# Kernel optimization log

Measured on AMD Instinct MI355X. Metric: run time of the kernel, lower is better.

The kernel has to match this reference:

```python
import jax, jax.numpy as jnp
import numpy as np

HEADS = 8
DIM_HEAD = 128
SCALE = DIM_HEAD ** -0.5
EPS = 1e-5


def layer_norm(t, w, b):
    mu = t.mean(-1, keepdims=True)
    var = ((t - mu) ** 2).mean(-1, keepdims=True)
    return (t - mu) * jax.lax.rsqrt(var + EPS) * w + b


def setup_inputs() -> dict:
    key = jax.random.key(0)
    ks = jax.random.split(key, 8)
    b, n, dim = 4, 1024, 1024
    inner = HEADS * DIM_HEAD  # 1024
    w = 0.02
    return {
        "x": jax.random.normal(ks[0], (b, n, dim), jnp.float32),
        "cond_info": jax.random.normal(ks[1], (b, n, dim), jnp.float32),
        "ref": jax.random.normal(ks[2], (b, n, dim), jnp.float32),
        "ln_w": jnp.ones((dim,), jnp.float32),
        "ln_b": jnp.zeros((dim,), jnp.float32),
        "cln_w": jnp.ones((dim,), jnp.float32),
        "cln_b": jnp.zeros((dim,), jnp.float32),
        "Wk": jax.random.normal(ks[3], (3 * dim, inner), jnp.float32) * w,
        "Wv": jax.random.normal(ks[4], (2 * dim, inner), jnp.float32) * w,
        "Wo": jax.random.normal(ks[5], (inner, dim), jnp.float32) * w,
        "bo": jnp.zeros((dim,), jnp.float32),
        "th_w": jax.random.normal(ks[6], (HEADS, HEADS), jnp.float32) * 0.3,
        "cth_w": jax.random.normal(ks[7], (HEADS, HEADS), jnp.float32) * 0.3,
    }


def reference(x, cond_info, ref, ln_w, ln_b, cln_w, cln_b, Wk, Wv, Wo, bo, th_w, cth_w):
    b, n, _ = x.shape
    h, d = HEADS, DIM_HEAD
    xn = layer_norm(x, ln_w, ln_b)
    rn = layer_norm(ref, ln_w, ln_b)
    cn = layer_norm(cond_info, cln_w, cln_b)
    # projections (y_to_q output is unused in the original forward; omitted)
    cond = jnp.concatenate([xn, cn, rn], axis=-1) @ Wk   # [b, n, h*d]
    refv = jnp.concatenate([xn, rn], axis=-1) @ Wv       # [b, n, h*d]
    split = lambda t: t.reshape(b, n, h, d).transpose(0, 2, 1, 3)  # b h n d
    cond, refv = split(cond), split(refv)
    sim = jnp.einsum('bhid,bhjd->bhij', cond, refv) * SCALE
    attn = jax.nn.softmax(sim, axis=-1)           # row softmax
    context_attn = jax.nn.softmax(sim, axis=-2)   # column softmax
    # talking heads: 1x1 conv over head dim, weight [out_h, in_h]
    attn = jnp.einsum('gh,bhij->bgij', th_w, attn)
    context_attn = jnp.einsum('gh,bhij->bgij', cth_w, context_attn)
    out = jnp.einsum('bhij,bhjd->bhid', attn, refv)
    context_out = jnp.einsum('bhji,bhjd->bhid', context_attn, cond)
    merge = lambda t: t.transpose(0, 2, 1, 3).reshape(b, n, h * d)
    out = merge(out) @ Wo + bo
    context_out = merge(context_out)
    return out, context_out
```

## Files before the change

kernel.cpp:

```cpp
#include <hip/hip_runtime.h>
#include <hip/hip_bf16.h>
#include <stdint.h>

typedef unsigned short u16;
typedef __attribute__((ext_vector_type(8))) short bf16x8;
typedef __attribute__((ext_vector_type(4))) float f32x4;

#define HEADS 8
#define DHEAD 128
#define NSEQ 1024
#define BATCH 4
#define DIM 1024
#define ATT_SCALE 0.088388347648318447f

static __device__ __forceinline__ float bf2f(u16 u){
  union { unsigned int i; float f; } c; c.i = ((unsigned int)u) << 16; return c.f;
}
static __device__ __forceinline__ u16 f2bf(float f){
  union { float f; unsigned int i; } c; c.f = f;
  unsigned int x = c.i;
  return (u16)((x + 0x7fffu + ((x >> 16) & 1u)) >> 16);
}

static __device__ __forceinline__ void gload_lds16(const void* g, void* l){
  __builtin_amdgcn_global_load_lds((__attribute__((address_space(1))) void*)(g),
                                   (__attribute__((address_space(3))) void*)(l),
                                   16, 0, 0);
}

__global__ __launch_bounds__(256)
void ln_kernel(const float* __restrict__ x, const float* __restrict__ w,
               const float* __restrict__ b, u16* __restrict__ out)
{
  const int row = blockIdx.x;
  const int t = threadIdx.x;
  const float* xr = x + (size_t)row * DIM;
  float4 v4 = *(const float4*)(xr + t*4);
  float v[4] = {v4.x, v4.y, v4.z, v4.w};
  float s = v[0]+v[1]+v[2]+v[3];
  __shared__ float red[256];
  red[t] = s; __syncthreads();
  for (int o=128;o;o>>=1){ if (t<o) red[t]+=red[t+o]; __syncthreads(); }
  const float mean = red[0] * (1.0f/DIM);
  __syncthreads();
  s = 0.f;
#pragma unroll
  for (int i=0;i<4;i++){ float d = v[i]-mean; s += d*d; }
  red[t] = s; __syncthreads();
  for (int o=128;o;o>>=1){ if (t<o) red[t]+=red[t+o]; __syncthreads(); }
  const float rstd = rsqrtf(red[0]*(1.0f/DIM) + 1e-5f);
  float4 w4 = *(const float4*)(w + t*4);
  float4 b4 = *(const float4*)(b + t*4);
  float wv[4] = {w4.x, w4.y, w4.z, w4.w};
  float bv[4] = {b4.x, b4.y, b4.z, b4.w};
  union { uint2 u; u16 s[4]; } ov;
#pragma unroll
  for (int i=0;i<4;i++)
    ov.s[i] = f2bf((v[i]-mean)*rstd*wv[i] + bv[i]);
  *(uint2*)(out + (size_t)row*DIM + t*4) = ov.u;
}

__global__ __launch_bounds__(256)
void wcvt_kernel(const float* __restrict__ Wk, const float* __restrict__ Wv,
                 const float* __restrict__ Wo,
                 u16* __restrict__ WkT, u16* __restrict__ WvT, u16* __restrict__ WoT)
{
  const int z = blockIdx.z;
  const int K = (z==0) ? 3072 : (z==1) ? 2048 : 1024;
  if ((int)blockIdx.x*32 >= K) return;
  const float* W = (z==0) ? Wk : (z==1) ? Wv : Wo;
  u16* WT = (z==0) ? WkT : (z==1) ? WvT : WoT;
  __shared__ float tile[32][33];
  const int k0 = blockIdx.x*32, n0 = blockIdx.y*32;
  const int t = threadIdx.x, tc = t&31, tr = t>>5;
#pragma unroll
  for (int p=0;p<4;p++)
    tile[tr+p*8][tc] = W[(size_t)(k0+tr+p*8)*DIM + n0+tc];
  __syncthreads();
#pragma unroll
  for (int p=0;p<4;p++)
    WT[(size_t)(n0+tr+p*8)*K + k0+tc] = f2bf(tile[tc][tr+p*8]);
}

__global__ __launch_bounds__(256)
void gemm_kernel(const u16* __restrict__ A0, const u16* __restrict__ A1,
                 const u16* __restrict__ A2, const u16* __restrict__ A0b,
                 const u16* __restrict__ A1b,
                 const u16* __restrict__ B1, const u16* __restrict__ B2,
                 void* __restrict__ Cv, void* __restrict__ Cv2,
                 const float* __restrict__ bias,
                 int K1, int K2, int lda, int ldb1, int ldb2, int ldc,
                 long a_plane, long b_plane, long c_plane,
                 int epi1, int epi2, int z_split, float alpha)
{
  __shared__ __attribute__((aligned(16))) u16 sA[2][4096];
  __shared__ __attribute__((aligned(16))) u16 sB[2][4096];
  const int t = threadIdx.x;
  const int m0 = blockIdx.y*128, n0 = blockIdx.x*128;
  const int zz = blockIdx.z;
  const bool side = (zz >= z_split);
  const int z = side ? (zz - z_split) : zz;
  const u16* a0 = (side ? A0b : A0) + (size_t)z*a_plane;
  const u16* a1 = (side ? A1b : A1) + (size_t)z*a_plane;
  const u16* a2 = A2 + (size_t)z*a_plane;
  const u16* bB = (side ? B2 : B1) + (size_t)z*b_plane;
  void* Cp = side ? Cv2 : Cv;
  const int EPI = side ? epi2 : epi1;
  const int K   = side ? K2 : K1;
  const int ldb = side ? ldb2 : ldb1;

  const int wave = t>>6, lane = t&63;
  const int wm = (wave>>1)*64, wn = (wave&1)*64;
  const int lm = lane&15, q = lane>>4;

  const f32x4 zero4 = {0.f,0.f,0.f,0.f};
  f32x4 acc[4][4];
#pragma unroll
  for (int i=0;i<4;i++)
#pragma unroll
    for (int j=0;j<4;j++) acc[i][j] = zero4;

  const int arowblk = wave*32;

  const int KT = K >> 5;

  auto issueA = [&](int kt, int buf){
    const int kg = kt<<5, seg = kg>>10, ka = kg&1023;
    const u16* Ap = (seg==0) ? a0 : (seg==1 ? a1 : a2);
#pragma unroll
    for (int rr=0; rr<2; ++rr){
      const int rb = arowblk + rr*16;
      gload_lds16(Ap + (size_t)(m0+rb+lm)*lda + (ka + q*8), &sA[buf][rb*32]);
    }
  };
  auto issueB = [&](int kt, int buf){
    const int kg = kt<<5;
#pragma unroll
    for (int rr=0; rr<2; ++rr){
      const int rb = arowblk + rr*16;
      gload_lds16(bB + (size_t)(n0+rb+lm)*ldb + (kg + q*8), &sB[buf][rb*32]);
    }
  };

  issueA(0, 0);
  issueB(0, 0);

  int cur = 0;
  for (int kt=0; kt<KT; ++kt){
    __syncthreads();
    if (kt+1 < KT){
      issueA(kt+1, cur^1);
      issueB(kt+1, cur^1);
    }
    bf16x8 af[4], bfr[4];
#pragma unroll
    for (int f=0; f<4; ++f){
      af[f]  = *(const bf16x8*)&sA[cur][((wm>>4)+f)*512 + lane*8];
      bfr[f] = *(const bf16x8*)&sB[cur][((wn>>4)+f)*512 + lane*8];
    }
#pragma unroll
    for (int fm=0; fm<4; ++fm)
#pragma unroll
      for (int fn=0; fn<4; ++fn)
        acc[fm][fn] = __builtin_amdgcn_mfma_f32_16x16x32_bf16(af[fm], bfr[fn], acc[fm][fn], 0, 0, 0);
    cur ^= 1;
  }

#pragma unroll
  for (int fm=0; fm<4; ++fm){
#pragma unroll
    for (int fn=0; fn<4; ++fn){
#pragma unroll
      for (int r=0; r<4; ++r){
        const int m = m0 + wm + fm*16 + q*4 + r;
        const int n = n0 + wn + fn*16 + lm;
        float val = acc[fm][fn][r] * alpha;
        if (EPI == 0){
          ((u16*)Cp)[(size_t)z*c_plane + (size_t)m*ldc + n] = f2bf(val);
        } else if (EPI == 1){
          ((u16*)Cp)[((size_t)(z>>3)*NSEQ + m)*DIM + (size_t)(z&7)*DHEAD + n] = f2bf(val);
        } else if (EPI == 2){
          ((float*)Cp)[(size_t)m*ldc + n] = val + bias[n];
        } else if (EPI == 3){
          ((u16*)Cp)[(size_t)(((m>>10)*HEADS + (n>>7))*NSEQ + (m&1023))*DHEAD + (n&127)] = f2bf(val);
        } else {
          ((float*)Cp)[((size_t)(z>>3)*NSEQ + m)*DIM + (size_t)(z&7)*DHEAD + n] = val;
        }
      }
    }
  }
}

__global__ __launch_bounds__(256)
void transpose_kernel(const u16* __restrict__ X, u16* __restrict__ XT)
{
  __shared__ u16 tile[32][33];
  const int z = blockIdx.z;
  const int i0 = blockIdx.y*32, d0 = blockIdx.x*32;
  const int t = threadIdx.x;
  const int tc = t & 31, tr = t >> 5;
  const u16* Xp = X + (size_t)z*NSEQ*DHEAD;
#pragma unroll
  for (int p=0;p<4;p++){
    int i = tr + p*8;
    tile[i][tc] = Xp[(size_t)(i0+i)*DHEAD + d0 + tc];
  }
  __syncthreads();
  u16* Op = XT + (size_t)z*DHEAD*NSEQ;
#pragma unroll
  for (int p=0;p<4;p++){
    int d = tr + p*8;
    Op[(size_t)(d0+d)*NSEQ + i0 + tc] = tile[tc][d];
  }
}

__global__ __launch_bounds__(256)
void row_stats_kernel(const u16* __restrict__ sim,
                      float* __restrict__ rmax, float* __restrict__ rrcp)
{
  const int wave = threadIdx.x >> 6, lane = threadIdx.x & 63;
  const int row = blockIdx.x*4 + wave;
  const u16* sr = sim + (size_t)row * NSEQ;
  float v[16]; float m = -1e30f;
#pragma unroll
  for (int c=0;c<16;c++){ v[c] = bf2f(sr[lane + c*64]); m = fmaxf(m, v[c]); }
#pragma unroll
  for (int off=32; off; off>>=1) m = fmaxf(m, __shfl_xor(m, off));
  float s = 0.f;
#pragma unroll
  for (int c=0;c<16;c++) s += __expf(v[c]-m);
#pragma unroll
  for (int off=32; off; off>>=1) s += __shfl_xor(s, off);
  if (lane == 0){ rmax[row] = m; rrcp[row] = 1.0f/s; }
}

__global__ __launch_bounds__(256)
void col_stats_kernel(const u16* __restrict__ sim,
                      float* __restrict__ cmax, float* __restrict__ crcp)
{
  __shared__ float smx[4][64], ssm[4][64];
  const int t = threadIdx.x;
  const int jl = t & 63, slice = t >> 6;
  const int c = blockIdx.x*64 + jl;
  const int bh = c >> 10, j = c & 1023;
  const u16* sp = sim + (size_t)bh*NSEQ*NSEQ + j + (size_t)(slice*256)*NSEQ;
  float m = -1e30f, s = 0.f;
  for (int i=0;i<256;i++){
    float v = bf2f(sp[(size_t)i*NSEQ]);
    float nm = fmaxf(m, v);
    s = s*__expf(m-nm) + __expf(v-nm);
    m = nm;
  }
  smx[slice][jl] = m; ssm[slice][jl] = s;
  __syncthreads();
  if (slice == 0){
    float M = smx[0][jl];
#pragma unroll
    for (int p=1;p<4;p++) M = fmaxf(M, smx[p][jl]);
    float S = 0.f;
#pragma unroll
    for (int p=0;p<4;p++) S += ssm[p][jl]*__expf(smx[p][jl]-M);
    cmax[c] = M; crcp[c] = 1.0f/S;
  }
}

__global__ __launch_bounds__(256)
void mix_kernel(u16* simam,
                const float* __restrict__ rmax, const float* __restrict__ rrcp,
                const float* __restrict__ cmax, const float* __restrict__ crcp,
                const float* __restrict__ thw, const float* __restrict__ cthw,
                u16* __restrict__ cmT)
{
  __shared__ float s_th[64], s_cth[64];
  __shared__ u16 s_cm[8][32][33];
  const int t = threadIdx.x;
  if (t < 64){ s_th[t] = thw[t]; s_cth[t] = cthw[t]; }
  __syncthreads();
  const int b = blockIdx.z, i0 = blockIdx.y*32, j0 = blockIdx.x*32;
  const int tj = t & 31, ti = t >> 5;
  for (int p=0;p<4;p++){
    const int i = ti + p*8;
    float a[8], c[8];
#pragma unroll
    for (int h=0;h<8;h++){
      const int bh = b*8 + h;
      const float v = bf2f(simam[((size_t)bh*NSEQ + (i0+i))*NSEQ + j0 + tj]);
      a[h] = __expf(v - rmax[(size_t)bh*NSEQ + i0+i]) * rrcp[(size_t)bh*NSEQ + i0+i];
      c[h] = __expf(v - cmax[(size_t)bh*NSEQ + j0+tj]) * crcp[(size_t)bh*NSEQ + j0+tj];
    }
#pragma unroll
    for (int g=0;g<8;g++){
      float sa = 0.f, sc = 0.f;
#pragma unroll
      for (int h=0;h<8;h++){ sa += s_th[g*8+h]*a[h]; sc += s_cth[g*8+h]*c[h]; }
      simam[((size_t)(b*8+g)*NSEQ + (i0+i))*NSEQ + j0 + tj] = f2bf(sa);
      s_cm[g][i][tj] = f2bf(sc);
    }
  }
  __syncthreads();
#pragma unroll
  for (int g=0;g<8;g++){
#pragma unroll
    for (int p=0;p<4;p++){
      const int j = ti + p*8;
      cmT[((size_t)(b*8+g)*NSEQ + (j0+j))*NSEQ + i0 + tj] = s_cm[g][tj][j];
    }
  }
}

extern "C" void kernel_launch(void* const* d_in, const int* in_sizes, int n_in,
                              void* d_out, int out_size, void* d_ws, size_t ws_size,
                              hipStream_t stream)
{
  const float* x     = (const float*)d_in[0];
  const float* cinfo = (const float*)d_in[1];
  const float* ref   = (const float*)d_in[2];
  const float* ln_w  = (const float*)d_in[3];
  const float* ln_b  = (const float*)d_in[4];
  const float* cln_w = (const float*)d_in[5];
  const float* cln_b = (const float*)d_in[6];
  const float* Wk    = (const float*)d_in[7];
  const float* Wv    = (const float*)d_in[8];
  const float* Wo    = (const float*)d_in[9];
  const float* bo    = (const float*)d_in[10];
  const float* thw   = (const float*)d_in[11];
  const float* cthw  = (const float*)d_in[12];
  float* out = (float*)d_out;

  char* ws = (char*)d_ws;
  u16* xn    = (u16*)(ws + 0);
  u16* cn    = (u16*)(ws + 8388608);
  u16* rn    = (u16*)(ws + 16777216);
  u16* cond  = (u16*)(ws + 25165824);
  u16* refv  = (u16*)(ws + 33554432);
  u16* condT = (u16*)(ws + 41943040);
  u16* refvT = (u16*)(ws + 50331648);
  u16* sim   = (u16*)(ws + 58720256);
  u16* cmT   = (u16*)(ws + 125829120);
  u16* WkT   = (u16*)(ws + 192937984);
  u16* WvT   = (u16*)(ws + 199229440);
  u16* WoT   = (u16*)(ws + 203423744);
  float* rmax = (float*)(ws + 8388608);
  float* rrcp = (float*)(ws + 8388608 + 131072);
  float* cmax = (float*)(ws + 8388608 + 262144);
  float* crcp = (float*)(ws + 8388608 + 393216);
  u16* out_pre = (u16*)(ws + 0);

  ln_kernel<<<4096, 256, 0, stream>>>(x,     ln_w,  ln_b,  xn);
  ln_kernel<<<4096, 256, 0, stream>>>(ref,   ln_w,  ln_b,  rn);
  ln_kernel<<<4096, 256, 0, stream>>>(cinfo, cln_w, cln_b, cn);

  wcvt_kernel<<<dim3(96,32,3), 256, 0, stream>>>(Wk, Wv, Wo, WkT, WvT, WoT);

  gemm_kernel<<<dim3(8,32,2), 256, 0, stream>>>(
      xn, cn, rn, xn, rn, WkT, WvT, cond, refv, nullptr,
      3072, 2048, DIM, 3072, 2048, 0, 0, 0, 0, 3, 3, 1, 1.0f);

  transpose_kernel<<<dim3(4,32,32), 256, 0, stream>>>(cond, condT);
  transpose_kernel<<<dim3(4,32,32), 256, 0, stream>>>(refv, refvT);

  gemm_kernel<<<dim3(8,8,32), 256, 0, stream>>>(
      cond, cond, cond, cond, cond, refv, refv, sim, sim, nullptr,
      DHEAD, DHEAD, DHEAD, DHEAD, DHEAD, NSEQ,
      (long)NSEQ*DHEAD, (long)NSEQ*DHEAD, (long)NSEQ*NSEQ, 0, 0, 1000000, ATT_SCALE);

  row_stats_kernel<<<8192, 256, 0, stream>>>(sim, rmax, rrcp);
  col_stats_kernel<<<512, 256, 0, stream>>>(sim, cmax, crcp);

  mix_kernel<<<dim3(32,32,4), 256, 0, stream>>>(sim, rmax, rrcp, cmax, crcp, thw, cthw, cmT);

  gemm_kernel<<<dim3(1,8,64), 256, 0, stream>>>(
      sim, sim, sim, cmT, cmT, refvT, condT, out_pre, out + (size_t)BATCH*NSEQ*DIM, nullptr,
      1024, 1024, NSEQ, NSEQ, NSEQ, 0,
      (long)NSEQ*NSEQ, (long)DHEAD*NSEQ, 0, 1, 4, 32, 1.0f);

  gemm_kernel<<<dim3(8,32,1), 256, 0, stream>>>(
      out_pre, out_pre, out_pre, out_pre, out_pre, WoT, WoT, out, out, bo,
      1024, 1024, DIM, 1024, 1024, DIM, 0, 0, 0, 2, 2, 1000000, 1.0f);
}
```

Measured before the change: 472.8 us.

## Store attention matrices and transposed values in k-panel layout for PV gemm

The mix kernel now writes the mixed row-attention and column-attention matrices into a separate buffer in a k-panelled layout (32-column panels stored contiguously), and the transpose kernel writes condT/refvT the same way. A templated PANEL gemm path then loads each 32-wide k-slice as a contiguous block instead of strided rows, aiming to improve load coalescing and cache locality in the large attention-times-value gemm. Workspace is reshuffled so WoT is converted later into the freed sim region, which adds an extra kernel launch and relies on the aliasing being correct.

```diff
diff --git a/kernel.cpp b/kernel.cpp
--- a/kernel.cpp
+++ b/kernel.cpp
@@ -61,15 +61,8 @@
 }
 
 __global__ __launch_bounds__(256)
-void wcvt_kernel(const float* __restrict__ Wk, const float* __restrict__ Wv,
-                 const float* __restrict__ Wo,
-                 u16* __restrict__ WkT, u16* __restrict__ WvT, u16* __restrict__ WoT)
-{
-  const int z = blockIdx.z;
-  const int K = (z==0) ? 3072 : (z==1) ? 2048 : 1024;
-  if ((int)blockIdx.x*32 >= K) return;
-  const float* W = (z==0) ? Wk : (z==1) ? Wv : Wo;
-  u16* WT = (z==0) ? WkT : (z==1) ? WvT : WoT;
+void wcvt_kernel(const float* __restrict__ W, u16* __restrict__ WT, int K)
+{
   __shared__ float tile[32][33];
   const int k0 = blockIdx.x*32, n0 = blockIdx.y*32;
   const int t = threadIdx.x, tc = t&31, tr = t>>5;
@@ -82,6 +75,7 @@
     WT[(size_t)(n0+tr+p*8)*K + k0+tc] = f2bf(tile[tc][tr+p*8]);
 }
 
+template<bool PANEL>
 __global__ __launch_bounds__(256)
 void gemm_kernel(const u16* __restrict__ A0, const u16* __restrict__ A1,
                  const u16* __restrict__ A2, const u16* __restrict__ A0b,
@@ -125,20 +119,39 @@
   const int KT = K >> 5;
 
   auto issueA = [&](int kt, int buf){
-    const int kg = kt<<5, seg = kg>>10, ka = kg&1023;
-    const u16* Ap = (seg==0) ? a0 : (seg==1 ? a1 : a2);
-#pragma unroll
-    for (int rr=0; rr<2; ++rr){
-      const int rb = arowblk + rr*16;
-      gload_lds16(Ap + (size_t)(m0+rb+lm)*lda + (ka + q*8), &sA[buf][rb*32]);
+    const int kg = kt<<5;
+    if (PANEL){
+#pragma unroll
+      for (int rr=0; rr<2; ++rr){
+        const int rb = arowblk + rr*16;
+        gload_lds16(a0 + (size_t)(kg>>5)*32768 + (size_t)(m0+rb+lm)*32 + q*8,
+                    &sA[buf][rb*32]);
+      }
+    } else {
+      const int seg = kg>>10, ka = kg&1023;
+      const u16* Ap = (seg==0) ? a0 : (seg==1 ? a1 : a2);
+#pragma unroll
+      for (int rr=0; rr<2; ++rr){
+        const int rb = arowblk + rr*16;
+        gload_lds16(Ap + (size_t)(m0+rb+lm)*lda + (ka + q*8), &sA[buf][rb*32]);
+      }
     }
   };
   auto issueB = [&](int kt, int buf){
     const int kg = kt<<5;
-#pragma unroll
-    for (int rr=0; rr<2; ++rr){
-      const int rb = arowblk + rr*16;
-      gload_lds16(bB + (size_t)(n0+rb+lm)*ldb + (kg + q*8), &sB[buf][rb*32]);
+    if (PANEL){
+#pragma unroll
+      for (int rr=0; rr<2; ++rr){
+        const int rb = arowblk + rr*16;
+        gload_lds16(bB + (size_t)(kg>>5)*4096 + (size_t)(n0+rb+lm)*32 + q*8,
+                    &sB[buf][rb*32]);
+      }
+    } else {
+#pragma unroll
+      for (int rr=0; rr<2; ++rr){
+        const int rb = arowblk + rr*16;
+        gload_lds16(bB + (size_t)(n0+rb+lm)*ldb + (kg + q*8), &sB[buf][rb*32]);
+      }
     }
   };
 
@@ -210,7 +223,7 @@
 #pragma unroll
   for (int p=0;p<4;p++){
     int d = tr + p*8;
-    Op[(size_t)(d0+d)*NSEQ + i0 + tc] = tile[tc][d];
+    Op[((size_t)(i0>>5)*(DHEAD*32) + (size_t)(d0+d)*32) + tc] = tile[tc][d];
   }
 }
 
@@ -265,11 +278,11 @@
 }
 
 __global__ __launch_bounds__(256)
-void mix_kernel(u16* simam,
+void mix_kernel(const u16* __restrict__ sim,
                 const float* __restrict__ rmax, const float* __restrict__ rrcp,
                 const float* __restrict__ cmax, const float* __restrict__ crcp,
                 const float* __restrict__ thw, const float* __restrict__ cthw,
-                u16* __restrict__ cmT)
+                u16* __restrict__ am, u16* __restrict__ cmT)
 {
   __shared__ float s_th[64], s_cth[64];
   __shared__ u16 s_cm[8][32][33];
@@ -284,7 +297,7 @@
 #pragma unroll
     for (int h=0;h<8;h++){
       const int bh = b*8 + h;
-      const float v = bf2f(simam[((size_t)bh*NSEQ + (i0+i))*NSEQ + j0 + tj]);
+      const float v = bf2f(sim[((size_t)bh*NSEQ + (i0+i))*NSEQ + j0 + tj]);
       a[h] = __expf(v - rmax[(size_t)bh*NSEQ + i0+i]) * rrcp[(size_t)bh*NSEQ + i0+i];
       c[h] = __expf(v - cmax[(size_t)bh*NSEQ + j0+tj]) * crcp[(size_t)bh*NSEQ + j0+tj];
     }
@@ -293,17 +306,19 @@
       float sa = 0.f, sc = 0.f;
 #pragma unroll
       for (int h=0;h<8;h++){ sa += s_th[g*8+h]*a[h]; sc += s_cth[g*8+h]*c[h]; }
-      simam[((size_t)(b*8+g)*NSEQ + (i0+i))*NSEQ + j0 + tj] = f2bf(sa);
+      am[(size_t)(b*8+g)*(NSEQ*NSEQ) + ((size_t)(j0>>5)*NSEQ + (i0+i))*32 + tj] = f2bf(sa);
       s_cm[g][i][tj] = f2bf(sc);
     }
   }
   __syncthreads();
+  const int a2 = t & 31, b2 = t >> 5;
 #pragma unroll
   for (int g=0;g<8;g++){
 #pragma unroll
     for (int p=0;p<4;p++){
-      const int j = ti + p*8;
-      cmT[((size_t)(b*8+g)*NSEQ + (j0+j))*NSEQ + i0 + tj] = s_cm[g][tj][j];
+      const int tjj = b2 + p*8;
+      cmT[(size_t)(b*8+g)*(NSEQ*NSEQ) + ((size_t)(i0>>5)*NSEQ + (j0+tjj))*32 + a2]
+        = s_cm[g][a2][tjj];
     }
   }
 }
@@ -336,10 +351,11 @@
   u16* condT = (u16*)(ws + 41943040);
   u16* refvT = (u16*)(ws + 50331648);
   u16* sim   = (u16*)(ws + 58720256);
-  u16* cmT   = (u16*)(ws + 125829120);
+  u16* am    = (u16*)(ws + 125829120);
+  u16* cmT   = (u16*)(ws + 192937984);
   u16* WkT   = (u16*)(ws + 192937984);
   u16* WvT   = (u16*)(ws + 199229440);
-  u16* WoT   = (u16*)(ws + 203423744);
+  u16* WoT   = (u16*)(ws + 58720256);
   float* rmax = (float*)(ws + 8388608);
   float* rrcp = (float*)(ws + 8388608 + 131072);
   float* cmax = (float*)(ws + 8388608 + 262144);
@@ -350,16 +366,17 @@
   ln_kernel<<<4096, 256, 0, stream>>>(ref,   ln_w,  ln_b,  rn);
   ln_kernel<<<4096, 256, 0, stream>>>(cinfo, cln_w, cln_b, cn);
 
-  wcvt_kernel<<<dim3(96,32,3), 256, 0, stream>>>(Wk, Wv, Wo, WkT, WvT, WoT);
-
-  gemm_kernel<<<dim3(8,32,2), 256, 0, stream>>>(
+  wcvt_kernel<<<dim3(96,32), 256, 0, stream>>>(Wk, WkT, 3072);
+  wcvt_kernel<<<dim3(64,32), 256, 0, stream>>>(Wv, WvT, 2048);
+
+  gemm_kernel<false><<<dim3(8,32,2), 256, 0, stream>>>(
       xn, cn, rn, xn, rn, WkT, WvT, cond, refv, nullptr,
       3072, 2048, DIM, 3072, 2048, 0, 0, 0, 0, 3, 3, 1, 1.0f);
 
   transpose_kernel<<<dim3(4,32,32), 256, 0, stream>>>(cond, condT);
   transpose_kernel<<<dim3(4,32,32), 256, 0, stream>>>(refv, refvT);
 
-  gemm_kernel<<<dim3(8,8,32), 256, 0, stream>>>(
+  gemm_kernel<false><<<dim3(8,8,32), 256, 0, stream>>>(
       cond, cond, cond, cond, cond, refv, refv, sim, sim, nullptr,
       DHEAD, DHEAD, DHEAD, DHEAD, DHEAD, NSEQ,
       (long)NSEQ*DHEAD, (long)NSEQ*DHEAD, (long)NSEQ*NSEQ, 0, 0, 1000000, ATT_SCALE);
@@ -367,14 +384,17 @@
   row_stats_kernel<<<8192, 256, 0, stream>>>(sim, rmax, rrcp);
   col_stats_kernel<<<512, 256, 0, stream>>>(sim, cmax, crcp);
 
-  mix_kernel<<<dim3(32,32,4), 256, 0, stream>>>(sim, rmax, rrcp, cmax, crcp, thw, cthw, cmT);
-
-  gemm_kernel<<<dim3(1,8,64), 256, 0, stream>>>(
-      sim, sim, sim, cmT, cmT, refvT, condT, out_pre, out + (size_t)BATCH*NSEQ*DIM, nullptr,
-      1024, 1024, NSEQ, NSEQ, NSEQ, 0,
+  mix_kernel<<<dim3(32,32,4), 256, 0, stream>>>(sim, rmax, rrcp, cmax, crcp,
+                                                thw, cthw, am, cmT);
+
+  wcvt_kernel<<<dim3(32,32), 256, 0, stream>>>(Wo, WoT, 1024);
+
+  gemm_kernel<true><<<dim3(1,8,64), 256, 0, stream>>>(
+      am, am, am, cmT, cmT, refvT, condT, out_pre, out + (size_t)BATCH*NSEQ*DIM, nullptr,
+      1024, 1024, 0, 0, 0, 0,
       (long)NSEQ*NSEQ, (long)DHEAD*NSEQ, 0, 1, 4, 32, 1.0f);
 
-  gemm_kernel<<<dim3(8,32,1), 256, 0, stream>>>(
+  gemm_kernel<false><<<dim3(8,32,1), 256, 0, stream>>>(
       out_pre, out_pre, out_pre, out_pre, out_pre, WoT, WoT, out, out, bo,
       1024, 1024, DIM, 1024, 1024, DIM, 0, 0, 0, 2, 2, 1000000, 1.0f);
 }
```

Result: slower. 571.5 us (+20.9%).
